# Kernel tuning notes

Hardware: AMD Instinct MI355X
Metric: run time of the kernel (lower is better)

Reference implementation:

```python
import jax, jax.numpy as jnp
import numpy as np

EMBED_DIMS = 192
NUM_HEADS = 6
WH, WW = 7, 7
N_TOK = WH * WW
B_WIN = 4096


def _rpe_index(Wh, Ww):
    coords = np.array([[x, y] for x in range(Ww) for y in range(Wh)])  # [N,2]
    d = coords[None, :, :] - coords[:, None, :]                        # [N,N,2]
    idx = (d[:, :, 0] + Ww - 1) * (2 * Ww - 1) + (d[:, :, 1] + Wh - 1)
    return idx.T  # transpose(0,1) as in the torch code


def setup_inputs() -> dict:
    key = jax.random.key(0)
    ks = jax.random.split(key, 6)
    C = EMBED_DIMS
    return {
        "x": jax.random.normal(ks[0], (B_WIN, N_TOK, C), dtype=jnp.float32),
        "qkv_w": jax.random.normal(ks[1], (3 * C, C), dtype=jnp.float32) * 0.02,
        "qkv_b": jax.random.normal(ks[2], (3 * C,), dtype=jnp.float32) * 0.02,
        "proj_w": jax.random.normal(ks[3], (C, C), dtype=jnp.float32) * 0.02,
        "proj_b": jax.random.normal(ks[4], (C,), dtype=jnp.float32) * 0.02,
        "rpe_table": jax.random.normal(ks[5], ((2 * WH - 1) * (2 * WW - 1), NUM_HEADS), dtype=jnp.float32),
        "rpe_idx": jnp.asarray(_rpe_index(WH, WW), dtype=jnp.int32),
    }


def reference(x, qkv_w, qkv_b, proj_w, proj_b, rpe_table, rpe_idx):
    B, N, C = x.shape
    H = NUM_HEADS
    hd = C // H
    scale = hd ** -0.5
    # qkv projection: torch Linear is x @ W.T + b
    qkv = x @ qkv_w.T + qkv_b                      # [B, N, 3C]
    qkv = qkv.reshape(B, N, 3, H, hd).transpose(2, 0, 3, 1, 4)  # [3, B, H, N, hd]
    q, k, v = qkv[0] * scale, qkv[1], qkv[2]
    attn = jnp.einsum("bhnd,bhmd->bhnm", q, k)     # [B, H, N, N]
    # relative position bias gather: table[idx] -> [N, N, H] -> [H, N, N]
    bias = rpe_table[rpe_idx].transpose(2, 0, 1)
    attn = jax.nn.softmax(attn + bias, axis=-1)
    out = jnp.einsum("bhnm,bhmd->bhnd", attn, v)   # [B, H, N, hd]
    out = out.transpose(0, 2, 1, 3).reshape(B, N, C)
    return out @ proj_w.T + proj_b
```

## Files before the change

### kernel.cpp

```cpp
#include <hip/hip_runtime.h>
#include <stdint.h>

#define NWIN 4096
#define NTOK 49
#define CDIM 192
#define NH   6
#define HD   32

typedef __attribute__((ext_vector_type(8))) short short8;
typedef __attribute__((ext_vector_type(4))) float floatx4;
typedef unsigned short ushort_t;
typedef unsigned int uint32;

#define XS_S 200
#define QK_S 296
#define P_S  72
#define VT_S 72

__device__ __forceinline__ ushort_t f2bf(float f) {
    uint32 u = __float_as_uint(f);
    u += 0x7fffu + ((u >> 16) & 1u);
    return (ushort_t)(u >> 16);
}

__global__ void wmsa_prologue(const float* __restrict__ qkv_w,
                              const float* __restrict__ proj_w,
                              const float* __restrict__ rpe_table,
                              const int*   __restrict__ rpe_idx,
                              ushort_t* __restrict__ qkv_wb,
                              ushort_t* __restrict__ proj_wb,
                              float* __restrict__ biasws)
{
    int i = blockIdx.x * 256 + threadIdx.x;
    if (i < 110592) {
        qkv_wb[i] = f2bf(qkv_w[i]);
    } else if (i < 147456) {
        proj_wb[i - 110592] = f2bf(proj_w[i - 110592]);
    } else if (i < 147456 + NH * NTOK * 64) {
        int r = i - 147456;
        int h = r / (NTOK * 64);
        int rem = r - h * (NTOK * 64);
        int n = rem >> 6, m = rem & 63;
        biasws[r] = (m < NTOK) ? rpe_table[rpe_idx[n * NTOK + m] * NH + h] : 0.f;
    }
}

__global__ __launch_bounds__(256)
void wmsa_mfma(const float* __restrict__ x,
               const ushort_t* __restrict__ qkv_wb,
               const float* __restrict__ qkv_b,
               const ushort_t* __restrict__ proj_wb,
               const float* __restrict__ proj_b,
               const float* __restrict__ biasws,
               float* __restrict__ out)
{
    __shared__ alignas(16) ushort_t reg0[NTOK * XS_S];
    __shared__ alignas(16) ushort_t qkvs[NTOK * QK_S];
    __shared__ alignas(16) ushort_t Pb[NTOK * P_S];
    __shared__ alignas(16) ushort_t Vt[HD * VT_S];

    const int b    = blockIdx.x;
    const int t    = threadIdx.x;
    const int w    = t >> 6;
    const int lane = t & 63;
    const int quad = lane >> 4;
    const int c    = lane & 15;
    const float scale = 0.17677669529663687f;

    const float* xb = x + (size_t)b * (NTOK * CDIM);

    for (int i = t; i < (NTOK * CDIM) / 4; i += 256) {
        int e = i * 4;
        int n = e / CDIM, d = e - n * CDIM;
        float4 v = *(const float4*)(xb + e);
        ushort_t* p = &reg0[n * XS_S + d];
        p[0] = f2bf(v.x); p[1] = f2bf(v.y); p[2] = f2bf(v.z); p[3] = f2bf(v.w);
    }
    __syncthreads();

    short8 afr[4][6];
    #pragma unroll
    for (int mt = 0; mt < 4; ++mt) {
        int row = mt * 16 + c;
        #pragma unroll
        for (int ks = 0; ks < 6; ++ks)
            afr[mt][ks] = *(const short8*)&reg0[row * XS_S + ks * 32 + quad * 8];
    }

    for (int pass = 0; pass < 2; ++pass) {
        for (int nt = w; nt < 18; nt += 4) {
            int s_idx = nt / 6;
            int rem   = nt - s_idx * 6;
            int hh    = rem >> 1;
            int half  = nt & 1;
            int jrow  = s_idx * CDIM + (3 * pass + hh) * HD + half * 16 + c;
            const ushort_t* bp = qkv_wb + jrow * CDIM + quad * 8;

            floatx4 z = {0.f, 0.f, 0.f, 0.f};
            floatx4 acc[4];
            #pragma unroll
            for (int mt = 0; mt < 4; ++mt) acc[mt] = z;

            #pragma unroll
            for (int ks = 0; ks < 6; ++ks) {
                short8 bf = *(const short8*)(bp + ks * 32);
                #pragma unroll
                for (int mt = 0; mt < 4; ++mt)
                    acc[mt] = __builtin_amdgcn_mfma_f32_16x16x32_bf16(
                        afr[mt][ks], bf, acc[mt], 0, 0, 0);
            }

            float bias = qkv_b[jrow];
            float mul  = (s_idx == 0) ? scale : 1.f;
            int ecol   = s_idx * 96 + hh * HD + half * 16 + c;
            #pragma unroll
            for (int mt = 0; mt < 4; ++mt) {
                #pragma unroll
                for (int r = 0; r < 4; ++r) {
                    int n = mt * 16 + quad * 4 + r;
                    if (n < NTOK)
                        qkvs[n * QK_S + ecol] = f2bf((acc[mt][r] + bias) * mul);
                }
            }
        }
        __syncthreads();

        for (int hh = 0; hh < 3; ++hh) {
            int h = pass * 3 + hh;

            short8 aq = *(const short8*)&qkvs[(w * 16 + c) * QK_S + hh * HD + quad * 8];
            floatx4 sacc[4];
            #pragma unroll
            for (int nt = 0; nt < 4; ++nt) {
                short8 bk = *(const short8*)&qkvs[(nt * 16 + c) * QK_S + 96 + hh * HD + quad * 8];
                floatx4 z = {0.f, 0.f, 0.f, 0.f};
                sacc[nt] = __builtin_amdgcn_mfma_f32_16x16x32_bf16(aq, bk, z, 0, 0, 0);
            }

            const float* bpb = biasws + h * (NTOK * 64);
            #pragma unroll
            for (int r = 0; r < 4; ++r) {
                int n  = w * 16 + quad * 4 + r;
                int nc = (n < NTOK) ? n : (NTOK - 1);
                float sv[4];
                #pragma unroll
                for (int nt = 0; nt < 4; ++nt) {
                    int col = nt * 16 + c;
                    float bias = bpb[nc * 64 + col];
                    sv[nt] = (col < NTOK) ? (sacc[nt][r] + bias) : -1e30f;
                }
                float m0 = fmaxf(fmaxf(sv[0], sv[1]), fmaxf(sv[2], sv[3]));
                m0 = fmaxf(m0, __shfl_xor(m0, 1));
                m0 = fmaxf(m0, __shfl_xor(m0, 2));
                m0 = fmaxf(m0, __shfl_xor(m0, 4));
                m0 = fmaxf(m0, __shfl_xor(m0, 8));
                float ex[4], s0 = 0.f;
                #pragma unroll
                for (int nt = 0; nt < 4; ++nt) { ex[nt] = __expf(sv[nt] - m0); s0 += ex[nt]; }
                s0 += __shfl_xor(s0, 1);
                s0 += __shfl_xor(s0, 2);
                s0 += __shfl_xor(s0, 4);
                s0 += __shfl_xor(s0, 8);
                float inv = 1.f / s0;
                if (n < NTOK) {
                    #pragma unroll
                    for (int nt = 0; nt < 4; ++nt)
                        Pb[n * P_S + nt * 16 + c] = f2bf(ex[nt] * inv);
                }
            }

            for (int i = t; i < HD * 64; i += 256) {
                int d = i >> 6, m = i & 63;
                Vt[d * VT_S + m] = (m < NTOK)
                    ? qkvs[m * QK_S + 192 + hh * HD + d] : (ushort_t)0;
            }
            __syncthreads();

            floatx4 z2 = {0.f, 0.f, 0.f, 0.f};
            floatx4 oacc[2]; oacc[0] = z2; oacc[1] = z2;
            #pragma unroll
            for (int ks = 0; ks < 2; ++ks) {
                short8 ap = *(const short8*)&Pb[(w * 16 + c) * P_S + ks * 32 + quad * 8];
                #pragma unroll
                for (int nt = 0; nt < 2; ++nt) {
                    short8 bv = *(const short8*)&Vt[(nt * 16 + c) * VT_S + ks * 32 + quad * 8];
                    oacc[nt] = __builtin_amdgcn_mfma_f32_16x16x32_bf16(ap, bv, oacc[nt], 0, 0, 0);
                }
            }
            #pragma unroll
            for (int nt = 0; nt < 2; ++nt) {
                #pragma unroll
                for (int r = 0; r < 4; ++r) {
                    int n = w * 16 + quad * 4 + r;
                    if (n < NTOK)
                        reg0[n * XS_S + h * HD + nt * 16 + c] = f2bf(oacc[nt][r]);
                }
            }
            __syncthreads();
        }
    }

    short8 aof[4][6];
    #pragma unroll
    for (int mt = 0; mt < 4; ++mt) {
        int row = mt * 16 + c;
        #pragma unroll
        for (int ks = 0; ks < 6; ++ks)
            aof[mt][ks] = *(const short8*)&reg0[row * XS_S + ks * 32 + quad * 8];
    }
    for (int nt = w; nt < 12; nt += 4) {
        int j = nt * 16 + c;
        const ushort_t* bp = proj_wb + j * CDIM + quad * 8;
        floatx4 z = {0.f, 0.f, 0.f, 0.f};
        floatx4 acc[4];
        #pragma unroll
        for (int mt = 0; mt < 4; ++mt) acc[mt] = z;
        #pragma unroll
        for (int ks = 0; ks < 6; ++ks) {
            short8 bf = *(const short8*)(bp + ks * 32);
            #pragma unroll
            for (int mt = 0; mt < 4; ++mt)
                acc[mt] = __builtin_amdgcn_mfma_f32_16x16x32_bf16(
                    aof[mt][ks], bf, acc[mt], 0, 0, 0);
        }
        float pb = proj_b[j];
        #pragma unroll
        for (int mt = 0; mt < 4; ++mt) {
            #pragma unroll
            for (int r = 0; r < 4; ++r) {
                int n = mt * 16 + quad * 4 + r;
                if (n < NTOK)
                    out[((size_t)b * NTOK + n) * CDIM + j] = acc[mt][r] + pb;
            }
        }
    }
}

extern "C" void kernel_launch(void* const* d_in, const int* in_sizes, int n_in,
                              void* d_out, int out_size, void* d_ws, size_t ws_size,
                              hipStream_t stream)
{
    const float* x      = (const float*)d_in[0];
    const float* qkv_w  = (const float*)d_in[1];
    const float* qkv_b  = (const float*)d_in[2];
    const float* proj_w = (const float*)d_in[3];
    const float* proj_b = (const float*)d_in[4];
    const float* rpe_t  = (const float*)d_in[5];
    const int*   rpe_i  = (const int*)d_in[6];
    float*       o      = (float*)d_out;

    ushort_t* qkv_wb  = (ushort_t*)d_ws;
    ushort_t* proj_wb = qkv_wb + 110592;
    float*    biasws  = (float*)((char*)d_ws + (110592 + 36864) * sizeof(ushort_t));

    int tot = 147456 + NH * NTOK * 64;
    wmsa_prologue<<<dim3((tot + 255) / 256), dim3(256), 0, stream>>>(
        qkv_w, proj_w, rpe_t, rpe_i, qkv_wb, proj_wb, biasws);
    wmsa_mfma<<<dim3(NWIN), dim3(256), 0, stream>>>(
        x, qkv_wb, qkv_b, proj_wb, proj_b, biasws, o);
}
```

Measured before the change: 593.6 us.

## Compute V transposed via MFMA, process two heads per pass, cut barriers

The QKV/attention loop now runs in three passes of two heads instead of two passes of three. V is produced directly in transposed layout by swapping the MFMA operands (weights as A, activations as B), which removes the per-head LDS transpose loop. Per-head __syncthreads are dropped because each wave only reads its own P rows. The qkv staging buffer shrinks, lowering LDS per block and possibly allowing more resident blocks, at the cost of an extra pass of QKV GEMM scheduling.

```diff
diff --git a/kernel.cpp b/kernel.cpp
--- a/kernel.cpp
+++ b/kernel.cpp
@@ -12,10 +12,10 @@
 typedef unsigned short ushort_t;
 typedef unsigned int uint32;
 
-#define XS_S 200
-#define QK_S 296
-#define P_S  72
-#define VT_S 72
+#define XS_S  200
+#define QK2_S 136
+#define P_S   72
+#define VT_S  72
 
 __device__ __forceinline__ ushort_t f2bf(float f) {
     uint32 u = __float_as_uint(f);
@@ -55,9 +55,9 @@
                float* __restrict__ out)
 {
     __shared__ alignas(16) ushort_t reg0[NTOK * XS_S];
-    __shared__ alignas(16) ushort_t qkvs[NTOK * QK_S];
-    __shared__ alignas(16) ushort_t Pb[NTOK * P_S];
-    __shared__ alignas(16) ushort_t Vt[HD * VT_S];
+    __shared__ alignas(16) ushort_t qkvs[NTOK * QK2_S];
+    __shared__ alignas(16) ushort_t Pb[64 * P_S];
+    __shared__ alignas(16) ushort_t Vt[64 * VT_S];
 
     const int b    = blockIdx.x;
     const int t    = threadIdx.x;
@@ -87,20 +87,19 @@
             afr[mt][ks] = *(const short8*)&reg0[row * XS_S + ks * 32 + quad * 8];
     }
 
-    for (int pass = 0; pass < 2; ++pass) {
-        for (int nt = w; nt < 18; nt += 4) {
-            int s_idx = nt / 6;
-            int rem   = nt - s_idx * 6;
-            int hh    = rem >> 1;
-            int half  = nt & 1;
-            int jrow  = s_idx * CDIM + (3 * pass + hh) * HD + half * 16 + c;
-            const ushort_t* bp = qkv_wb + jrow * CDIM + quad * 8;
+    for (int pass = 0; pass < 3; ++pass) {
+        for (int e = w; e < 8; e += 4) {
+            int s_idx = e >> 2;
+            int hh    = (e >> 1) & 1;
+            int half  = e & 1;
+            int h     = pass * 2 + hh;
+            int jrow  = s_idx * CDIM + h * HD + half * 16 + c;
+            const ushort_t* bp = qkv_wb + (size_t)jrow * CDIM + quad * 8;
 
             floatx4 z = {0.f, 0.f, 0.f, 0.f};
             floatx4 acc[4];
             #pragma unroll
             for (int mt = 0; mt < 4; ++mt) acc[mt] = z;
-
             #pragma unroll
             for (int ks = 0; ks < 6; ++ks) {
                 short8 bf = *(const short8*)(bp + ks * 32);
@@ -109,30 +108,55 @@
                     acc[mt] = __builtin_amdgcn_mfma_f32_16x16x32_bf16(
                         afr[mt][ks], bf, acc[mt], 0, 0, 0);
             }
-
             float bias = qkv_b[jrow];
             float mul  = (s_idx == 0) ? scale : 1.f;
-            int ecol   = s_idx * 96 + hh * HD + half * 16 + c;
+            int ecol   = s_idx * 64 + hh * 32 + half * 16 + c;
             #pragma unroll
             for (int mt = 0; mt < 4; ++mt) {
                 #pragma unroll
                 for (int r = 0; r < 4; ++r) {
                     int n = mt * 16 + quad * 4 + r;
                     if (n < NTOK)
-                        qkvs[n * QK_S + ecol] = f2bf((acc[mt][r] + bias) * mul);
-                }
+                        qkvs[n * QK2_S + ecol] = f2bf((acc[mt][r] + bias) * mul);
+                }
+            }
+        }
+
+        for (int vt = w; vt < 16; vt += 4) {
+            int hh    = vt >> 3;
+            int dtile = (vt >> 2) & 1;
+            int ttile = vt & 3;
+            int h     = pass * 2 + hh;
+            const ushort_t* ap = qkv_wb
+                + (size_t)(2 * CDIM + h * HD + dtile * 16 + c) * CDIM + quad * 8;
+
+            floatx4 acc = {0.f, 0.f, 0.f, 0.f};
+            #pragma unroll
+            for (int ks = 0; ks < 6; ++ks) {
+                short8 af = *(const short8*)(ap + ks * 32);
+                acc = __builtin_amdgcn_mfma_f32_16x16x32_bf16(
+                    af, afr[ttile][ks], acc, 0, 0, 0);
+            }
+            int tok = ttile * 16 + c;
+            #pragma unroll
+            for (int r = 0; r < 4; ++r) {
+                int d = dtile * 16 + quad * 4 + r;
+                float bias = qkv_b[2 * CDIM + h * HD + d];
+                Vt[(hh * HD + d) * VT_S + tok] =
+                    (tok < NTOK) ? f2bf(acc[r] + bias) : (ushort_t)0;
             }
         }
         __syncthreads();
 
-        for (int hh = 0; hh < 3; ++hh) {
-            int h = pass * 3 + hh;
-
-            short8 aq = *(const short8*)&qkvs[(w * 16 + c) * QK_S + hh * HD + quad * 8];
+        for (int hh = 0; hh < 2; ++hh) {
+            int h = pass * 2 + hh;
+
+            short8 aq = *(const short8*)&qkvs[(w * 16 + c) * QK2_S + hh * 32 + quad * 8];
             floatx4 sacc[4];
             #pragma unroll
             for (int nt = 0; nt < 4; ++nt) {
-                short8 bk = *(const short8*)&qkvs[(nt * 16 + c) * QK_S + 96 + hh * HD + quad * 8];
+                short8 bk = *(const short8*)
+                    &qkvs[(nt * 16 + c) * QK2_S + 64 + hh * 32 + quad * 8];
                 floatx4 z = {0.f, 0.f, 0.f, 0.f};
                 sacc[nt] = __builtin_amdgcn_mfma_f32_16x16x32_bf16(aq, bk, z, 0, 0, 0);
             }
@@ -169,13 +193,6 @@
                 }
             }
 
-            for (int i = t; i < HD * 64; i += 256) {
-                int d = i >> 6, m = i & 63;
-                Vt[d * VT_S + m] = (m < NTOK)
-                    ? qkvs[m * QK_S + 192 + hh * HD + d] : (ushort_t)0;
-            }
-            __syncthreads();
-
             floatx4 z2 = {0.f, 0.f, 0.f, 0.f};
             floatx4 oacc[2]; oacc[0] = z2; oacc[1] = z2;
             #pragma unroll
@@ -183,7 +200,8 @@
                 short8 ap = *(const short8*)&Pb[(w * 16 + c) * P_S + ks * 32 + quad * 8];
                 #pragma unroll
                 for (int nt = 0; nt < 2; ++nt) {
-                    short8 bv = *(const short8*)&Vt[(nt * 16 + c) * VT_S + ks * 32 + quad * 8];
+                    short8 bv = *(const short8*)
+                        &Vt[(hh * HD + nt * 16 + c) * VT_S + ks * 32 + quad * 8];
                     oacc[nt] = __builtin_amdgcn_mfma_f32_16x16x32_bf16(ap, bv, oacc[nt], 0, 0, 0);
                 }
             }
@@ -196,8 +214,8 @@
                         reg0[n * XS_S + h * HD + nt * 16 + c] = f2bf(oacc[nt][r]);
                 }
             }
-            __syncthreads();
-        }
+        }
+        __syncthreads();
     }
 
     short8 aof[4][6];
@@ -210,7 +228,7 @@
     }
     for (int nt = w; nt < 12; nt += 4) {
         int j = nt * 16 + c;
-        const ushort_t* bp = proj_wb + j * CDIM + quad * 8;
+        const ushort_t* bp = proj_wb + (size_t)j * CDIM + quad * 8;
         floatx4 z = {0.f, 0.f, 0.f, 0.f};
         floatx4 acc[4];
         #pragma unroll
```

Result: slower. 883.4 us (+48.8%).
